# Performance work log

Measured on AMD Instinct MI355X. Metric: run time of the kernel, lower is better.

The kernel has to match this reference:

```python
import jax, jax.numpy as jnp
import numpy as np

B, T, C, H = 2, 2048, 1024, 16
HS = C // H  # head_size = 64
EPS = 1e-5


def _ln(x, g, b):
    m = jnp.mean(x, axis=-1, keepdims=True)
    v = jnp.mean(jnp.square(x - m), axis=-1, keepdims=True)
    return (x - m) * jax.lax.rsqrt(v + EPS) * g + b


def setup_inputs() -> dict:
    key = jax.random.key(0)
    ks = jax.random.split(key, 16)
    s = lambda k, shape, fan: jax.random.normal(k, shape, jnp.float32) * (fan ** -0.5)
    return {
        "x": jax.random.normal(ks[0], (B, T, C), jnp.float32),
        "Wq": s(ks[1], (H, C, HS), C), "bq": jnp.zeros((H, HS), jnp.float32),
        "Wk": s(ks[2], (H, C, HS), C), "bk": jnp.zeros((H, HS), jnp.float32),
        "Wv": s(ks[3], (H, C, HS), C), "bv": jnp.zeros((H, HS), jnp.float32),
        "Wo": s(ks[4], (C, C), C), "bo": jnp.zeros((C,), jnp.float32),
        "g1": jnp.ones((C,), jnp.float32), "b1": jnp.zeros((C,), jnp.float32),
        "g2": jnp.ones((C,), jnp.float32), "b2": jnp.zeros((C,), jnp.float32),
        "W1": s(ks[5], (C, C), C), "bf1": jnp.zeros((C,), jnp.float32),
        "W2": s(ks[6], (C, C), C), "bf2": jnp.zeros((C,), jnp.float32),
    }


def _block(x, Wq, bq, Wk, bk, Wv, bv, Wo, bo, g1, b1, g2, b2, W1, bf1, W2, bf2):
    h = _ln(x, g1, b1)
    # per-head projections, batched over heads: (B,T,C) x (H,C,HS) -> (B,H,T,HS)
    q = jnp.einsum('btc,hcd->bhtd', h, Wq) + bq[None, :, None, :]
    k = jnp.einsum('btc,hcd->bhtd', h, Wk) + bk[None, :, None, :]
    v = jnp.einsum('btc,hcd->bhtd', h, Wv) + bv[None, :, None, :]
    w = jnp.einsum('bhqd,bhkd->bhqk', q, k) * (HS ** -0.5)
    causal = jnp.tril(jnp.ones((T, T), bool))  # tril[q,k]==0 -> -inf
    w = jnp.where(causal[None, None], w, -jnp.inf)
    # FAITHFUL quirk: original uses F.softmax(w, dim=1) on (B,T,T),
    # i.e. normalization over the QUERY axis (axis=2 of bhqk).
    w = jax.nn.softmax(w, axis=2)
    att = jnp.einsum('bhqk,bhkd->bhqd', w, v)
    att = att.transpose(0, 2, 1, 3).reshape(x.shape[0], x.shape[1], -1)  # concat heads
    x = x + att @ Wo + bo
    h2 = _ln(x, g2, b2)
    x = x + jax.nn.relu(h2 @ W1 + bf1) @ W2 + bf2
    return x


def reference(x, Wq, bq, Wk, bk, Wv, bv, Wo, bo, g1, b1, g2, b2, W1, bf1, W2, bf2):
    return _block(x, Wq, bq, Wk, bk, Wv, bv, Wo, bo, g1, b1, g2, b2, W1, bf1, W2, bf2)
```

## Files before the change

### kernel.cpp

```cpp
#include <hip/hip_runtime.h>
#include <hip/hip_bf16.h>
#include <math.h>


#define B_   2
#define T_   2048
#define C_   1024
#define H_   16
#define HS_  64
#define NROWS 4096
#define C3   3072
#define K1C  0.1803368801111244f

typedef unsigned short ushort_t;
typedef __attribute__((ext_vector_type(8))) short short8;
typedef __attribute__((ext_vector_type(4))) float f32x4;
typedef __attribute__((ext_vector_type(16))) float f32x16;

__device__ __forceinline__ ushort_t f2bf(float f) {
  __hip_bfloat16 h = __float2bfloat16(f);
  ushort_t u; __builtin_memcpy(&u, &h, 2); return u;
}
__device__ __forceinline__ float bf2f(ushort_t u) {
  union { unsigned u; float f; } v; v.u = ((unsigned)u) << 16;
  return v.f;
}
__device__ __forceinline__ unsigned pkhw(float a, float b) {
  unsigned u;
  asm("v_cvt_pk_bf16_f32 %0, %1, %2" : "=v"(u) : "v"(a), "v"(b));
  return u;
}
__device__ __forceinline__ short8 mk8(unsigned a, unsigned b, unsigned c, unsigned d) {
  union { unsigned u[4]; short8 s; } t;
  t.u[0] = a; t.u[1] = b; t.u[2] = c; t.u[3] = d; return t.s;
}
__device__ __forceinline__ void pl32swap(unsigned &a, unsigned &b) {
  asm("v_permlane32_swap_b32 %0, %1" : "+v"(a), "+v"(b));
}
__device__ __forceinline__ f32x4 mfma16(short8 a, short8 b, f32x4 c) {
  return __builtin_amdgcn_mfma_f32_16x16x32_bf16(a, b, c, 0, 0, 0);
}
__device__ __forceinline__ f32x16 mfma32(short8 a, short8 b, f32x16 c) {
  return __builtin_amdgcn_mfma_f32_32x32x16_bf16(a, b, c, 0, 0, 0);
}
typedef const __attribute__((address_space(1))) void g_void;
typedef __attribute__((address_space(3))) void l_void;
__device__ __forceinline__ void gl_lds16(const void* g, void* l) {
  __builtin_amdgcn_global_load_lds((g_void*)g, (l_void*)l, 16, 0, 0);
}

__global__ __launch_bounds__(256) void ln_bf16(
    const float* __restrict__ x, const float* __restrict__ g,
    const float* __restrict__ b, ushort_t* __restrict__ out) {
  int row = blockIdx.x;
  const float* xr = x + (size_t)row * C_;
  int t = threadIdx.x;
  float4 v = ((const float4*)xr)[t];
  float s  = v.x + v.y + v.z + v.w;
  float ss = v.x*v.x + v.y*v.y + v.z*v.z + v.w*v.w;
  #pragma unroll
  for (int off = 32; off > 0; off >>= 1) {
    s  += __shfl_down(s, off);
    ss += __shfl_down(ss, off);
  }
  __shared__ float red[2][4];
  int wid = t >> 6, lane = t & 63;
  if (lane == 0) { red[0][wid] = s; red[1][wid] = ss; }
  __syncthreads();
  if (t == 0) {
    float a = 0, c = 0;
    for (int i = 0; i < 4; i++) { a += red[0][i]; c += red[1][i]; }
    red[0][0] = a; red[1][0] = c;
  }
  __syncthreads();
  float mean = red[0][0] * (1.0f / C_);
  float var  = red[1][0] * (1.0f / C_) - mean * mean;
  float r = rsqrtf(var + 1e-5f);
  float4 gv = ((const float4*)g)[t];
  float4 bv = ((const float4*)b)[t];
  ushort4 o;
  o.x = f2bf((v.x - mean) * r * gv.x + bv.x);
  o.y = f2bf((v.y - mean) * r * gv.y + bv.y);
  o.z = f2bf((v.z - mean) * r * gv.z + bv.z);
  o.w = f2bf((v.w - mean) * r * gv.w + bv.w);
  ((ushort4*)(out + (size_t)row * C_))[t] = o;
}

__global__ __launch_bounds__(256) void prep_weights(
    const float* __restrict__ Wq, const float* __restrict__ Wk,
    const float* __restrict__ Wv, const float* __restrict__ Wo,
    const float* __restrict__ W1, const float* __restrict__ W2,
    const float* __restrict__ bq, const float* __restrict__ bk,
    const float* __restrict__ bv, ushort_t* __restrict__ Wqkvt,
    ushort_t* __restrict__ Wot3, float* __restrict__ bqkv) {
  int bid = blockIdx.x;
  if (bid < 12288) {
    int idx = bid * 256 + threadIdx.x;
    int n = idx >> 10, c = idx & 1023;
    int sel = n >> 10, nn = n & 1023;
    const float* W = (sel == 0) ? Wq : ((sel == 1) ? Wk : Wv);
    Wqkvt[idx] = f2bf(W[((size_t)(nn >> 6) * C_ + c) * HS_ + (nn & 63)]);
  } else if (bid < 24576) {
    int idx = (bid - 12288) * 256 + threadIdx.x;
    int sel = idx >> 20, rem = idx & 1048575;
    int n = rem >> 10, k = rem & 1023;
    const float* W = (sel == 0) ? Wo : ((sel == 1) ? W1 : W2);
    Wot3[idx] = f2bf(W[(size_t)k * C_ + n]);
  } else {
    int i = (bid - 24576) * 256 + threadIdx.x;
    if (i < 3072)
      bqkv[i] = (i < 1024) ? bq[i] : ((i < 2048) ? bk[i - 1024] : bv[i - 2048]);
  }
}

__global__ __launch_bounds__(256) void gemm128q(
    const ushort_t* __restrict__ A, const ushort_t* __restrict__ Bt,
    const float* __restrict__ bias, ushort_t* __restrict__ Cm,
    int M, int N, int K) {
  __shared__ ushort_t As[128 * 32];
  __shared__ ushort_t Bs[128 * 32];
  int t = threadIdx.x;
  int bid = blockIdx.x;
  int xcd = bid & 7, loc = bid >> 3;
  int mb = (xcd >> 1) * 8 + (loc & 7);
  int nb = (xcd & 1) * 12 + (loc >> 3);
  int m0 = mb * 128, n0 = nb * 128;
  int w = t >> 6, l = t & 63;
  int wr = w >> 1, wc = w & 1;
  int lo = l & 15, hi = l >> 4;
  f32x4 acc[4][4] = {};
  int srow = t >> 2, scol = (t & 3) * 8;
  const ushort_t* Ag = A  + (size_t)(m0 + srow) * K + scol;
  const ushort_t* Bg = Bt + (size_t)(n0 + srow) * K + scol;
  ushort_t* AsP = As + t * 8;
  ushort_t* BsP = Bs + t * 8;
  for (int k0 = 0; k0 < K; k0 += 32) {
    gl_lds16(Ag + k0,          AsP);
    gl_lds16(Ag + 64 * K + k0, AsP + 64 * 32);
    gl_lds16(Bg + k0,          BsP);
    gl_lds16(Bg + 64 * K + k0, BsP + 64 * 32);
    __syncthreads();
    short8 af[4], bfr[4];
    #pragma unroll
    for (int i = 0; i < 4; i++)
      af[i] = *(const short8*)&As[(wr * 64 + i * 16 + lo) * 32 + hi * 8];
    #pragma unroll
    for (int j = 0; j < 4; j++)
      bfr[j] = *(const short8*)&Bs[(wc * 64 + j * 16 + lo) * 32 + hi * 8];
    #pragma unroll
    for (int i = 0; i < 4; i++)
      #pragma unroll
      for (int j = 0; j < 4; j++)
        acc[i][j] = mfma16(af[i], bfr[j], acc[i][j]);
    __syncthreads();
  }
  float qs = (n0 < C_) ? K1C : 1.0f;
  #pragma unroll
  for (int i = 0; i < 4; i++) {
    int m = m0 + wr * 64 + i * 16 + hi * 4;
    #pragma unroll
    for (int j = 0; j < 4; j++) {
      int n = n0 + wc * 64 + j * 16 + lo;
      float bv = bias[n];
      #pragma unroll
      for (int r = 0; r < 4; r++)
        Cm[(size_t)(m + r) * N + n] = f2bf((acc[i][j][r] + bv) * qs);
    }
  }
}

template<int OUT_BF16, int RELU, int HAS_RES>
__global__ __launch_bounds__(256) void gemm64(
    const ushort_t* __restrict__ A, const ushort_t* __restrict__ Bt,
    const float* __restrict__ bias, const float* __restrict__ res,
    void* __restrict__ Cm, int M, int N, int K) {
  __shared__ ushort_t As[128 * 32];
  __shared__ ushort_t Bs[64 * 32];
  int t = threadIdx.x;
  int m0 = blockIdx.y * 128, n0 = blockIdx.x * 64;
  int w = t >> 6, l = t & 63;
  int wr = w >> 1, wc = w & 1;
  int lo = l & 15, hi = l >> 4;
  f32x4 acc[4][2] = {};
  int srow = t >> 2, scol = (t & 3) * 8;
  const ushort_t* Ag = A  + (size_t)(m0 + srow) * K + scol;
  const ushort_t* Bg = Bt + (size_t)(n0 + srow) * K + scol;
  ushort_t* AsP = As + t * 8;
  ushort_t* BsP = Bs + t * 8;
  for (int k0 = 0; k0 < K; k0 += 32) {
    gl_lds16(Ag + k0,          AsP);
    gl_lds16(Ag + 64 * K + k0, AsP + 64 * 32);
    gl_lds16(Bg + k0,          BsP);
    __syncthreads();
    short8 af[4], bfr[2];
    #pragma unroll
    for (int i = 0; i < 4; i++)
      af[i] = *(const short8*)&As[(wr * 64 + i * 16 + lo) * 32 + hi * 8];
    #pragma unroll
    for (int j = 0; j < 2; j++)
      bfr[j] = *(const short8*)&Bs[(wc * 32 + j * 16 + lo) * 32 + hi * 8];
    #pragma unroll
    for (int i = 0; i < 4; i++)
      #pragma unroll
      for (int j = 0; j < 2; j++)
        acc[i][j] = mfma16(af[i], bfr[j], acc[i][j]);
    __syncthreads();
  }
  #pragma unroll
  for (int i = 0; i < 4; i++) {
    int m = m0 + wr * 64 + i * 16 + hi * 4;
    #pragma unroll
    for (int j = 0; j < 2; j++) {
      int n = n0 + wc * 32 + j * 16 + lo;
      float bv = bias[n];
      #pragma unroll
      for (int r = 0; r < 4; r++) {
        float v = acc[i][j][r] + bv;
        if (HAS_RES) v += res[(size_t)(m + r) * N + n];
        if (RELU) v = fmaxf(v, 0.f);
        if (OUT_BF16) ((ushort_t*)Cm)[(size_t)(m + r) * N + n] = f2bf(v);
        else          ((float*)Cm)[(size_t)(m + r) * N + n] = v;
      }
    }
  }
}

__global__ __launch_bounds__(256) void attn_stats(
    const ushort_t* __restrict__ QKV, float* __restrict__ dinv) {
  int bid = blockIdx.x;
  int xcd = bid & 7, loc = (bid >> 3) & 31, half = bid >> 8;
  int bh = xcd * 4 + (loc & 3);
  int j = loc >> 2;
  int kb = half ? (15 - j) : j;
  int b = bh >> 4, h = bh & 15;
  int t = threadIdx.x, w = t >> 6, l = t & 63, l31 = l & 31, hi32 = l >> 5;
  __shared__ ushort_t Qs[2][2][2048];
  const ushort_t* Qb = QKV + (size_t)b * T_ * C3 + h * HS_;
  const ushort_t* Kb = Qb + C_;
  int k0w = kb * 128 + w * 32;
  short8 ka[4];
  #pragma unroll
  for (int c = 0; c < 4; c++)
    ka[c] = *(const short8*)(Kb + (size_t)(k0w + l31) * C3 + c * 16 + hi32 * 8);
  float s[16];
  #pragma unroll
  for (int r = 0; r < 16; r++) s[r] = 0.f;

  int qoff[4];
  #pragma unroll
  for (int c = 0; c < 4; c++)
    qoff[c] = l31 * 64 + ((c * 2 + hi32) ^ (l31 & 7)) * 8;

  int sr = t >> 3, slot = t & 7, su = slot ^ (sr & 7);
  const ushort_t* Qsrc = Qb + (size_t)sr * C3 + su * 8;
  int qt0 = kb * 4, cnt = 64 - qt0;
  int dqt = qt0 + w;

  gl_lds16(Qsrc + (size_t)qt0 * 32 * C3,       &Qs[0][0][t * 8]);
  gl_lds16(Qsrc + (size_t)(qt0 + 1) * 32 * C3, &Qs[0][1][t * 8]);
  for (int i = 0; i < cnt; i += 2) {
    int buf = (i >> 1) & 1;
    if (i + 2 < cnt) {
      gl_lds16(Qsrc + (size_t)(qt0 + i + 2) * 32 * C3, &Qs[buf ^ 1][0][t * 8]);
      gl_lds16(Qsrc + (size_t)(qt0 + i + 3) * 32 * C3, &Qs[buf ^ 1][1][t * 8]);
      asm volatile("s_waitcnt vmcnt(2)");
    } else {
      asm volatile("s_waitcnt vmcnt(0)");
    }
    __builtin_amdgcn_s_barrier();
    __builtin_amdgcn_sched_barrier(0);
    #pragma unroll
    for (int sub = 0; sub < 2; sub++) {
      int qt = qt0 + i + sub;
      if (qt >= dqt) {
        const ushort_t* base = &Qs[buf][sub][0];
        short8 qf[4];
        #pragma unroll
        for (int c = 0; c < 4; c++)
          qf[c] = *(const short8*)(base + qoff[c]);
        __builtin_amdgcn_s_setprio(1);
        f32x16 d = {};
        #pragma unroll
        for (int c = 0; c < 4; c++) d = mfma32(ka[c], qf[c], d);
        __builtin_amdgcn_s_setprio(0);
        if (qt == dqt) {
          int qq = qt * 32 + l31;
          #pragma unroll
          for (int r = 0; r < 16; r++) {
            int k = k0w + (r & 3) + 8 * (r >> 2) + 4 * hi32;
            s[r] += (qq >= k) ? __builtin_amdgcn_exp2f(d[r]) : 0.f;
          }
        } else {
          #pragma unroll
          for (int r = 0; r < 16; r++) s[r] += __builtin_amdgcn_exp2f(d[r]);
        }
      }
    }
    __builtin_amdgcn_sched_barrier(0);
    __builtin_amdgcn_s_barrier();
    __builtin_amdgcn_sched_barrier(0);
  }
  #pragma unroll
  for (int off = 1; off < 32; off <<= 1)
    #pragma unroll
    for (int r = 0; r < 16; r++)
      s[r] += __shfl_xor(s[r], off);
  if (l31 == 0) {
    #pragma unroll
    for (int r = 0; r < 16; r++) {
      int k = k0w + (r & 3) + 8 * (r >> 2) + 4 * hi32;
      dinv[(size_t)bh * T_ + k] = 1.0f / s[r];
    }
  }
}

__global__ __launch_bounds__(256) void transpose_v(
    const ushort_t* __restrict__ QKV, const float* __restrict__ dinv,
    ushort_t* __restrict__ Vt) {
  int t0 = blockIdx.x * 64;
  int bh = blockIdx.y; int b = bh >> 4, h = bh & 15;
  __shared__ ushort_t tile[64][65];
  int tid = threadIdx.x;
  #pragma unroll
  for (int i = 0; i < 16; i++) {
    int idx = i * 256 + tid;
    int tt = idx >> 6, dd = idx & 63;
    float v = bf2f(QKV[(size_t)(b * T_ + t0 + tt) * C3 + 2 * C_ + h * HS_ + dd]);
    tile[tt][dd] = f2bf(v * dinv[(size_t)bh * T_ + t0 + tt]);
  }
  __syncthreads();
  #pragma unroll
  for (int i = 0; i < 16; i++) {
    int idx = i * 256 + tid;
    int dd = idx >> 6, tt = idx & 63;
    Vt[((size_t)(bh * HS_ + dd)) * T_ + t0 + tt] = tile[tt][dd];
  }
}

__global__ __launch_bounds__(256) void attn_pv(
    const ushort_t* __restrict__ QKV, const ushort_t* __restrict__ Vt,
    ushort_t* __restrict__ att) {
  int bid = blockIdx.x;
  int xcd = bid & 7, loc = (bid >> 3) & 31, half = bid >> 8;
  int bh = xcd * 4 + (loc & 3);
  int j = loc >> 2;
  int qb = half ? j : (15 - j);
  int b = bh >> 4, h = bh & 15;
  int t = threadIdx.x, w = t >> 6, l = t & 63, l31 = l & 31, hi32 = l >> 5;
  __shared__ ushort_t KV[2][2][2][2048];
  const ushort_t* Qb = QKV + (size_t)b * T_ * C3 + h * HS_;
  const ushort_t* Kb = Qb + C_;
  const ushort_t* Vb = Vt + (size_t)bh * HS_ * T_;
  int q0w = qb * 128 + w * 32;
  short8 qf[4];
  #pragma unroll
  for (int c = 0; c < 4; c++)
    qf[c] = *(const short8*)(Qb + (size_t)(q0w + l31) * C3 + c * 16 + hi32 * 8);
  f32x16 o0 = {}, o1 = {};
  int nkt = qb * 4 + 4;
  int dkt = q0w >> 5;

  int koff[4], voff[4];
  #pragma unroll
  for (int c = 0; c < 4; c++)
    koff[c] = l31 * 64 + ((c * 2 + hi32) ^ (l31 & 7)) * 8;
  #pragma unroll
  for (int i = 0; i < 4; i++) {
    int u = (i & 1) * 4 + (i >> 1) * 2 + hi32;
    voff[i] = 2048 + l31 * 64 + (u ^ (l31 & 7)) * 8;
  }

  int sr = t >> 3, slot = t & 7, su = slot ^ (sr & 7);
  int vdh = su >> 2, vc2 = su & 3;
  const ushort_t* Ksrc = Kb + (size_t)sr * C3 + su * 8;
  const ushort_t* Vsrc = Vb + (size_t)(vdh * 32 + sr) * T_ + vc2 * 8;

  gl_lds16(Ksrc,                  &KV[0][0][0][t * 8]);
  gl_lds16(Vsrc,                  &KV[0][0][1][t * 8]);
  gl_lds16(Ksrc + (size_t)32 * C3, &KV[0][1][0][t * 8]);
  gl_lds16(Vsrc + 32,             &KV[0][1][1][t * 8]);
  for (int kt = 0; kt < nkt; kt += 2) {
    int buf = (kt >> 1) & 1;
    if (kt + 2 < nkt) {
      gl_lds16(Ksrc + (size_t)(kt + 2) * 32 * C3, &KV[buf ^ 1][0][0][t * 8]);
      gl_lds16(Vsrc + (kt + 2) * 32,              &KV[buf ^ 1][0][1][t * 8]);
      gl_lds16(Ksrc + (size_t)(kt + 3) * 32 * C3, &KV[buf ^ 1][1][0][t * 8]);
      gl_lds16(Vsrc + (kt + 3) * 32,              &KV[buf ^ 1][1][1][t * 8]);
      asm volatile("s_waitcnt vmcnt(4)");
    } else {
      asm volatile("s_waitcnt vmcnt(0)");
    }
    __builtin_amdgcn_s_barrier();
    __builtin_amdgcn_sched_barrier(0);
    #pragma unroll
    for (int sub = 0; sub < 2; sub++) {
      int kts = kt + sub;
      if (kts <= dkt) {
        const ushort_t* base = &KV[buf][sub][0][0];
        short8 ka[4], vf[4];
        #pragma unroll
        for (int c = 0; c < 4; c++)
          ka[c] = *(const short8*)(base + koff[c]);
        #pragma unroll
        for (int i = 0; i < 4; i++)
          vf[i] = *(const short8*)(base + voff[i]);
        __builtin_amdgcn_s_setprio(1);
        f32x16 sacc = {};
        #pragma unroll
        for (int c = 0; c < 4; c++) sacc = mfma32(ka[c], qf[c], sacc);
        __builtin_amdgcn_s_setprio(0);
        float e[16];
        if (kts == dkt) {
          int qq = q0w + l31;
          #pragma unroll
          for (int r = 0; r < 16; r++) {
            int k = kts * 32 + (r & 3) + 8 * (r >> 2) + 4 * hi32;
            e[r] = (k <= qq) ? __builtin_amdgcn_exp2f(sacc[r]) : 0.f;
          }
        } else {
          #pragma unroll
          for (int r = 0; r < 16; r++) e[r] = __builtin_amdgcn_exp2f(sacc[r]);
        }
        unsigned u[8];
        #pragma unroll
        for (int j2 = 0; j2 < 8; j2++) u[j2] = pkhw(e[2 * j2], e[2 * j2 + 1]);
        pl32swap(u[0], u[2]); pl32swap(u[1], u[3]);
        pl32swap(u[4], u[6]); pl32swap(u[5], u[7]);
        short8 pa0 = mk8(u[0], u[1], u[2], u[3]);
        short8 pa1 = mk8(u[4], u[5], u[6], u[7]);
        __builtin_amdgcn_s_setprio(1);
        o0 = mfma32(pa0, vf[0], o0);
        o1 = mfma32(pa0, vf[1], o1);
        o0 = mfma32(pa1, vf[2], o0);
        o1 = mfma32(pa1, vf[3], o1);
        __builtin_amdgcn_s_setprio(0);
      }
    }
    __builtin_amdgcn_sched_barrier(0);
    __builtin_amdgcn_s_barrier();
    __builtin_amdgcn_sched_barrier(0);
  }

  #pragma unroll
  for (int r = 0; r < 16; r++) {
    int qq = q0w + (r & 3) + 8 * (r >> 2) + 4 * hi32;
    size_t base = (size_t)(b * T_ + qq) * C_ + h * HS_;
    att[base + l31]      = f2bf(o0[r]);
    att[base + 32 + l31] = f2bf(o1[r]);
  }
}

extern "C" void kernel_launch(void* const* d_in, const int* in_sizes, int n_in,
                              void* d_out, int out_size, void* d_ws, size_t ws_size,
                              hipStream_t stream) {
  const float* x   = (const float*)d_in[0];
  const float* Wq  = (const float*)d_in[1];
  const float* bq  = (const float*)d_in[2];
  const float* Wk  = (const float*)d_in[3];
  const float* bk  = (const float*)d_in[4];
  const float* Wv  = (const float*)d_in[5];
  const float* bv  = (const float*)d_in[6];
  const float* Wo  = (const float*)d_in[7];
  const float* bo  = (const float*)d_in[8];
  const float* g1  = (const float*)d_in[9];
  const float* b1  = (const float*)d_in[10];
  const float* g2  = (const float*)d_in[11];
  const float* b2  = (const float*)d_in[12];
  const float* W1  = (const float*)d_in[13];
  const float* bf1 = (const float*)d_in[14];
  const float* W2  = (const float*)d_in[15];
  const float* bf2 = (const float*)d_in[16];
  float* out = (float*)d_out;

  char* base = (char*)d_ws;
  const size_t MB = 1 << 20;
  ushort_t* QKVb  = (ushort_t*)(base);
  ushort_t* hb    = (ushort_t*)(base + 24 * MB);
  ushort_t* Vt    = (ushort_t*)(base + 32 * MB);
  float*    y     = (float*)   (base + 40 * MB);
  ushort_t* Wqkvt = (ushort_t*)(base + 56 * MB);
  ushort_t* Wot   = (ushort_t*)(base + 62 * MB);
  ushort_t* W1t   = (ushort_t*)(base + 64 * MB);
  ushort_t* W2t   = (ushort_t*)(base + 66 * MB);
  float*    bqkv  = (float*)   (base + 68 * MB);
  float*    dinv  = (float*)   (base + 68 * MB + 65536);

  prep_weights<<<24588, 256, 0, stream>>>(Wq, Wk, Wv, Wo, W1, W2,
                                          bq, bk, bv, Wqkvt, Wot, bqkv);

  ln_bf16<<<NROWS, 256, 0, stream>>>(x, g1, b1, hb);

  gemm128q<<<768, 256, 0, stream>>>(hb, Wqkvt, bqkv, QKVb, NROWS, C3, C_);

  attn_stats<<<512, 256, 0, stream>>>(QKVb, dinv);
  transpose_v<<<dim3(T_ / 64, 32), 256, 0, stream>>>(QKVb, dinv, Vt);
  ushort_t* attb = hb;
  attn_pv<<<512, 256, 0, stream>>>(QKVb, Vt, attb);

  dim3 g64(C_ / 64, NROWS / 128);
  gemm64<0,0,1><<<g64, 256, 0, stream>>>(attb, Wot, bo, x, y, NROWS, C_, C_);

  ushort_t* h2b = QKVb;
  ln_bf16<<<NROWS, 256, 0, stream>>>(y, g2, b2, h2b);
  ushort_t* f1b = Vt;
  gemm64<1,1,0><<<g64, 256, 0, stream>>>(h2b, W1t, bf1, nullptr, f1b, NROWS, C_, C_);
  gemm64<0,0,1><<<g64, 256, 0, stream>>>(f1b, W2t, bf2, y, out, NROWS, C_, C_);
}
```

Measured before the change: 210.4 us.

## Deepen GEMM K-tiles with swizzled LDS and widen attention prefetch stages

Both GEMM kernels now stage 64-wide K tiles instead of 32, with an XOR-swizzled LDS layout so fragment reads avoid bank conflicts. This halves the number of barrier pairs per K sweep. The attention stats and PV kernels now prefetch four 32-row tiles per stage instead of two, which cuts barriers and deepens the load pipeline. In exchange the kernels use more LDS, which may lower occupancy, and issue more loads in flight.

```diff
diff --git a/kernel.cpp b/kernel.cpp
--- a/kernel.cpp
+++ b/kernel.cpp
@@ -117,8 +117,8 @@
     const ushort_t* __restrict__ A, const ushort_t* __restrict__ Bt,
     const float* __restrict__ bias, ushort_t* __restrict__ Cm,
     int M, int N, int K) {
-  __shared__ ushort_t As[128 * 32];
-  __shared__ ushort_t Bs[128 * 32];
+  __shared__ ushort_t As[128 * 64];
+  __shared__ ushort_t Bs[128 * 64];
   int t = threadIdx.x;
   int bid = blockIdx.x;
   int xcd = bid & 7, loc = bid >> 3;
@@ -129,29 +129,39 @@
   int wr = w >> 1, wc = w & 1;
   int lo = l & 15, hi = l >> 4;
   f32x4 acc[4][4] = {};
-  int srow = t >> 2, scol = (t & 3) * 8;
-  const ushort_t* Ag = A  + (size_t)(m0 + srow) * K + scol;
-  const ushort_t* Bg = Bt + (size_t)(n0 + srow) * K + scol;
-  ushort_t* AsP = As + t * 8;
-  ushort_t* BsP = Bs + t * 8;
-  for (int k0 = 0; k0 < K; k0 += 32) {
-    gl_lds16(Ag + k0,          AsP);
-    gl_lds16(Ag + 64 * K + k0, AsP + 64 * 32);
-    gl_lds16(Bg + k0,          BsP);
-    gl_lds16(Bg + 64 * K + k0, BsP + 64 * 32);
+  int srow = t >> 3, ssw = (t & 7) ^ (srow & 7);
+  const ushort_t* Ag = A  + (size_t)(m0 + srow) * K + ssw * 8;
+  const ushort_t* Bg = Bt + (size_t)(n0 + srow) * K + ssw * 8;
+  int aoff[4][2], boff[4][2];
+  #pragma unroll
+  for (int i = 0; i < 4; i++)
+    #pragma unroll
+    for (int kk = 0; kk < 2; kk++) {
+      aoff[i][kk] = (wr * 64 + i * 16 + lo) * 64 + ((kk * 4 + hi) ^ (lo & 7)) * 8;
+      boff[i][kk] = (wc * 64 + i * 16 + lo) * 64 + ((kk * 4 + hi) ^ (lo & 7)) * 8;
+    }
+  for (int k0 = 0; k0 < K; k0 += 64) {
+    #pragma unroll
+    for (int i = 0; i < 4; i++) {
+      gl_lds16(Ag + (size_t)(i * 32) * K + k0, &As[i * 2048 + t * 8]);
+      gl_lds16(Bg + (size_t)(i * 32) * K + k0, &Bs[i * 2048 + t * 8]);
+    }
     __syncthreads();
-    short8 af[4], bfr[4];
+    short8 af[4][2], bfr[4][2];
     #pragma unroll
     for (int i = 0; i < 4; i++)
-      af[i] = *(const short8*)&As[(wr * 64 + i * 16 + lo) * 32 + hi * 8];
-    #pragma unroll
-    for (int j = 0; j < 4; j++)
-      bfr[j] = *(const short8*)&Bs[(wc * 64 + j * 16 + lo) * 32 + hi * 8];
-    #pragma unroll
-    for (int i = 0; i < 4; i++)
-      #pragma unroll
-      for (int j = 0; j < 4; j++)
-        acc[i][j] = mfma16(af[i], bfr[j], acc[i][j]);
+      #pragma unroll
+      for (int kk = 0; kk < 2; kk++) {
+        af[i][kk]  = *(const short8*)&As[aoff[i][kk]];
+        bfr[i][kk] = *(const short8*)&Bs[boff[i][kk]];
+      }
+    #pragma unroll
+    for (int kk = 0; kk < 2; kk++)
+      #pragma unroll
+      for (int i = 0; i < 4; i++)
+        #pragma unroll
+        for (int j = 0; j < 4; j++)
+          acc[i][j] = mfma16(af[i][kk], bfr[j][kk], acc[i][j]);
     __syncthreads();
   }
   float qs = (n0 < C_) ? K1C : 1.0f;
@@ -174,36 +184,54 @@
     const ushort_t* __restrict__ A, const ushort_t* __restrict__ Bt,
     const float* __restrict__ bias, const float* __restrict__ res,
     void* __restrict__ Cm, int M, int N, int K) {
-  __shared__ ushort_t As[128 * 32];
-  __shared__ ushort_t Bs[64 * 32];
+  __shared__ ushort_t As[128 * 64];
+  __shared__ ushort_t Bs[64 * 64];
   int t = threadIdx.x;
   int m0 = blockIdx.y * 128, n0 = blockIdx.x * 64;
   int w = t >> 6, l = t & 63;
   int wr = w >> 1, wc = w & 1;
   int lo = l & 15, hi = l >> 4;
   f32x4 acc[4][2] = {};
-  int srow = t >> 2, scol = (t & 3) * 8;
-  const ushort_t* Ag = A  + (size_t)(m0 + srow) * K + scol;
-  const ushort_t* Bg = Bt + (size_t)(n0 + srow) * K + scol;
-  ushort_t* AsP = As + t * 8;
-  ushort_t* BsP = Bs + t * 8;
-  for (int k0 = 0; k0 < K; k0 += 32) {
-    gl_lds16(Ag + k0,          AsP);
-    gl_lds16(Ag + 64 * K + k0, AsP + 64 * 32);
-    gl_lds16(Bg + k0,          BsP);
+  int srow = t >> 3, ssw = (t & 7) ^ (srow & 7);
+  const ushort_t* Ag = A  + (size_t)(m0 + srow) * K + ssw * 8;
+  const ushort_t* Bg = Bt + (size_t)(n0 + srow) * K + ssw * 8;
+  int aoff[4][2], boff[2][2];
+  #pragma unroll
+  for (int i = 0; i < 4; i++)
+    #pragma unroll
+    for (int kk = 0; kk < 2; kk++)
+      aoff[i][kk] = (wr * 64 + i * 16 + lo) * 64 + ((kk * 4 + hi) ^ (lo & 7)) * 8;
+  #pragma unroll
+  for (int j = 0; j < 2; j++)
+    #pragma unroll
+    for (int kk = 0; kk < 2; kk++)
+      boff[j][kk] = (wc * 32 + j * 16 + lo) * 64 + ((kk * 4 + hi) ^ (lo & 7)) * 8;
+  for (int k0 = 0; k0 < K; k0 += 64) {
+    #pragma unroll
+    for (int i = 0; i < 4; i++)
+      gl_lds16(Ag + (size_t)(i * 32) * K + k0, &As[i * 2048 + t * 8]);
+    #pragma unroll
+    for (int i = 0; i < 2; i++)
+      gl_lds16(Bg + (size_t)(i * 32) * K + k0, &Bs[i * 2048 + t * 8]);
     __syncthreads();
-    short8 af[4], bfr[2];
+    short8 af[4][2], bfr[2][2];
     #pragma unroll
     for (int i = 0; i < 4; i++)
-      af[i] = *(const short8*)&As[(wr * 64 + i * 16 + lo) * 32 + hi * 8];
+      #pragma unroll
+      for (int kk = 0; kk < 2; kk++)
+        af[i][kk] = *(const short8*)&As[aoff[i][kk]];
     #pragma unroll
     for (int j = 0; j < 2; j++)
-      bfr[j] = *(const short8*)&Bs[(wc * 32 + j * 16 + lo) * 32 + hi * 8];
-    #pragma unroll
-    for (int i = 0; i < 4; i++)
-      #pragma unroll
-      for (int j = 0; j < 2; j++)
-        acc[i][j] = mfma16(af[i], bfr[j], acc[i][j]);
+      #pragma unroll
+      for (int kk = 0; kk < 2; kk++)
+        bfr[j][kk] = *(const short8*)&Bs[boff[j][kk]];
+    #pragma unroll
+    for (int kk = 0; kk < 2; kk++)
+      #pragma unroll
+      for (int i = 0; i < 4; i++)
+        #pragma unroll
+        for (int j = 0; j < 2; j++)
+          acc[i][j] = mfma16(af[i][kk], bfr[j][kk], acc[i][j]);
     __syncthreads();
   }
   #pragma unroll
@@ -234,7 +262,7 @@
   int kb = half ? (15 - j) : j;
   int b = bh >> 4, h = bh & 15;
   int t = threadIdx.x, w = t >> 6, l = t & 63, l31 = l & 31, hi32 = l >> 5;
-  __shared__ ushort_t Qs[2][2][2048];
+  __shared__ ushort_t Qs[2][4][2048];
   const ushort_t* Qb = QKV + (size_t)b * T_ * C3 + h * HS_;
   const ushort_t* Kb = Qb + C_;
   int k0w = kb * 128 + w * 32;
@@ -256,21 +284,24 @@
   int qt0 = kb * 4, cnt = 64 - qt0;
   int dqt = qt0 + w;
 
-  gl_lds16(Qsrc + (size_t)qt0 * 32 * C3,       &Qs[0][0][t * 8]);
-  gl_lds16(Qsrc + (size_t)(qt0 + 1) * 32 * C3, &Qs[0][1][t * 8]);
-  for (int i = 0; i < cnt; i += 2) {
-    int buf = (i >> 1) & 1;
-    if (i + 2 < cnt) {
-      gl_lds16(Qsrc + (size_t)(qt0 + i + 2) * 32 * C3, &Qs[buf ^ 1][0][t * 8]);
-      gl_lds16(Qsrc + (size_t)(qt0 + i + 3) * 32 * C3, &Qs[buf ^ 1][1][t * 8]);
-      asm volatile("s_waitcnt vmcnt(2)");
+  #pragma unroll
+  for (int sub = 0; sub < 4; sub++)
+    gl_lds16(Qsrc + (size_t)(qt0 + sub) * 32 * C3, &Qs[0][sub][t * 8]);
+  for (int i = 0; i < cnt; i += 4) {
+    int buf = (i >> 2) & 1;
+    if (i + 4 < cnt) {
+      #pragma unroll
+      for (int sub = 0; sub < 4; sub++)
+        gl_lds16(Qsrc + (size_t)(qt0 + i + 4 + sub) * 32 * C3,
+                 &Qs[buf ^ 1][sub][t * 8]);
+      asm volatile("s_waitcnt vmcnt(4)");
     } else {
       asm volatile("s_waitcnt vmcnt(0)");
     }
     __builtin_amdgcn_s_barrier();
     __builtin_amdgcn_sched_barrier(0);
     #pragma unroll
-    for (int sub = 0; sub < 2; sub++) {
+    for (int sub = 0; sub < 4; sub++) {
       int qt = qt0 + i + sub;
       if (qt >= dqt) {
         const ushort_t* base = &Qs[buf][sub][0];
@@ -347,7 +378,7 @@
   int qb = half ? j : (15 - j);
   int b = bh >> 4, h = bh & 15;
   int t = threadIdx.x, w = t >> 6, l = t & 63, l31 = l & 31, hi32 = l >> 5;
-  __shared__ ushort_t KV[2][2][2][2048];
+  __shared__ ushort_t KV[2][4][2][2048];
   const ushort_t* Qb = QKV + (size_t)b * T_ * C3 + h * HS_;
   const ushort_t* Kb = Qb + C_;
   const ushort_t* Vb = Vt + (size_t)bh * HS_ * T_;
@@ -375,25 +406,27 @@
   const ushort_t* Ksrc = Kb + (size_t)sr * C3 + su * 8;
   const ushort_t* Vsrc = Vb + (size_t)(vdh * 32 + sr) * T_ + vc2 * 8;
 
-  gl_lds16(Ksrc,                  &KV[0][0][0][t * 8]);
-  gl_lds16(Vsrc,                  &KV[0][0][1][t * 8]);
-  gl_lds16(Ksrc + (size_t)32 * C3, &KV[0][1][0][t * 8]);
-  gl_lds16(Vsrc + 32,             &KV[0][1][1][t * 8]);
-  for (int kt = 0; kt < nkt; kt += 2) {
-    int buf = (kt >> 1) & 1;
-    if (kt + 2 < nkt) {
-      gl_lds16(Ksrc + (size_t)(kt + 2) * 32 * C3, &KV[buf ^ 1][0][0][t * 8]);
-      gl_lds16(Vsrc + (kt + 2) * 32,              &KV[buf ^ 1][0][1][t * 8]);
-      gl_lds16(Ksrc + (size_t)(kt + 3) * 32 * C3, &KV[buf ^ 1][1][0][t * 8]);
-      gl_lds16(Vsrc + (kt + 3) * 32,              &KV[buf ^ 1][1][1][t * 8]);
-      asm volatile("s_waitcnt vmcnt(4)");
+  #pragma unroll
+  for (int sub = 0; sub < 4; sub++) {
+    gl_lds16(Ksrc + (size_t)sub * 32 * C3, &KV[0][sub][0][t * 8]);
+    gl_lds16(Vsrc + sub * 32,              &KV[0][sub][1][t * 8]);
+  }
+  for (int kt = 0; kt < nkt; kt += 4) {
+    int buf = (kt >> 2) & 1;
+    if (kt + 4 < nkt) {
+      #pragma unroll
+      for (int sub = 0; sub < 4; sub++) {
+        gl_lds16(Ksrc + (size_t)(kt + 4 + sub) * 32 * C3, &KV[buf ^ 1][sub][0][t * 8]);
+        gl_lds16(Vsrc + (kt + 4 + sub) * 32,              &KV[buf ^ 1][sub][1][t * 8]);
+      }
+      asm volatile("s_waitcnt vmcnt(8)");
     } else {
       asm volatile("s_waitcnt vmcnt(0)");
     }
     __builtin_amdgcn_s_barrier();
     __builtin_amdgcn_sched_barrier(0);
     #pragma unroll
-    for (int sub = 0; sub < 2; sub++) {
+    for (int sub = 0; sub < 4; sub++) {
       int kts = kt + sub;
       if (kts <= dkt) {
         const ushort_t* base = &KV[buf][sub][0][0];
```

Result: faster. 204.4 us (-2.9%).
